# Kernel optimization log

Measured on AMD Instinct MI355X. Metric: run time of the kernel, lower is better.

The kernel has to match this reference:

```python
import jax, jax.numpy as jnp
import numpy as np


def setup_inputs() -> dict:
    key = jax.random.key(0)
    k1, k2, k3 = jax.random.split(key, 3)
    B, C, H, W, R = 4, 64, 128, 128, 16
    h_prev = jax.random.normal(k1, (B, C, H, W, R), dtype=jnp.float32)
    flow = jax.random.normal(k2, (B, 2, H, W), dtype=jnp.float32)
    dt = jax.random.uniform(k3, (B,), dtype=jnp.float32)
    return {"h_prev": h_prev, "flow": flow, "dt": dt}


def _bilinear_sample(img, ix, iy):
    # img: [K,H,W]; ix,iy: [H,W] unnormalized pixel coords, pre-clamped to
    # [0, W-1] / [0, H-1] (PyTorch grid_sample padding_mode='border').
    H, W = img.shape[-2], img.shape[-1]
    x0 = jnp.floor(ix)
    y0 = jnp.floor(iy)
    wx = ix - x0  # [H,W]
    wy = iy - y0
    x0i = jnp.clip(x0.astype(jnp.int32), 0, W - 1)
    x1i = jnp.clip(x0i + 1, 0, W - 1)
    y0i = jnp.clip(y0.astype(jnp.int32), 0, H - 1)
    y1i = jnp.clip(y0i + 1, 0, H - 1)
    v00 = img[:, y0i, x0i]  # [K,H,W]
    v01 = img[:, y0i, x1i]
    v10 = img[:, y1i, x0i]
    v11 = img[:, y1i, x1i]
    top = v00 * (1.0 - wx) + v01 * wx
    bot = v10 * (1.0 - wx) + v11 * wx
    return top * (1.0 - wy) + bot * wy


def reference(h_prev, flow, dt):
    B, C, H, W, R = h_prev.shape
    # base grid in normalized [-1,1] coords (torch.linspace endpoints)
    base_x = jnp.linspace(-1.0, 1.0, W, dtype=h_prev.dtype)[None, :]  # [1,W]
    base_y = jnp.linspace(-1.0, 1.0, H, dtype=h_prev.dtype)[:, None]  # [H,1]
    dtb = dt[:, None, None]  # [B,1,1]
    gx = base_x - flow[:, 0] * dtb  # [B,H,W] normalized x sample coords
    gy = base_y - flow[:, 1] * dtb  # [B,H,W]
    # unnormalize with align_corners=False, then border-clamp
    ix = jnp.clip(((gx + 1.0) * W - 1.0) * 0.5, 0.0, W - 1.0)
    iy = jnp.clip(((gy + 1.0) * H - 1.0) * 0.5, 0.0, H - 1.0)
    # grid is shared across R, so fold R into channels and sample once per batch
    img = jnp.moveaxis(h_prev, 4, 2).reshape(B, C * R, H, W)
    out = jax.vmap(_bilinear_sample)(img, ix, iy)  # [B, C*R, H, W]
    return jnp.moveaxis(out.reshape(B, C, R, H, W), 2, 4)  # [B,C,H,W,R]
```

## Files before the change

kernel.cpp:

```cpp
#include <hip/hip_runtime.h>


constexpr int B = 4, C = 64, H = 128, W = 128, R = 16;

__global__ __launch_bounds__(256) void lie_transport_kernel(
    const float* __restrict__ h_prev,
    const float* __restrict__ flow,
    const float* __restrict__ dt,
    float* __restrict__ out) {
  const int tid = blockIdx.x * 256 + threadIdx.x;
  const int r4  = (tid & 3) * 4;
  const int pix = tid >> 2;
  const int x = pix & (W - 1);
  const int y = (pix >> 7) & (H - 1);
  const int b = pix >> 14;

  const float dtb = dt[b];
  const float* fl = flow + (size_t)b * 2 * H * W;
  const float f0 = fl[y * W + x];
  const float f1 = fl[H * W + y * W + x];

  const float bx = -1.0f + 2.0f * (float)x / (float)(W - 1);
  const float by = -1.0f + 2.0f * (float)y / (float)(H - 1);
  const float gx = bx - f0 * dtb;
  const float gy = by - f1 * dtb;
  float ix = ((gx + 1.0f) * (float)W - 1.0f) * 0.5f;
  float iy = ((gy + 1.0f) * (float)H - 1.0f) * 0.5f;
  ix = fminf(fmaxf(ix, 0.0f), (float)(W - 1));
  iy = fminf(fmaxf(iy, 0.0f), (float)(H - 1));

  const float x0f = floorf(ix);
  const float y0f = floorf(iy);
  const float wx = ix - x0f;
  const float wy = iy - y0f;
  const int x0 = min(max((int)x0f, 0), W - 1);
  const int x1 = min(x0 + 1, W - 1);
  const int y0 = min(max((int)y0f, 0), H - 1);
  const int y1 = min(y0 + 1, H - 1);

  const float w00 = (1.0f - wx) * (1.0f - wy);
  const float w01 = wx * (1.0f - wy);
  const float w10 = (1.0f - wx) * wy;
  const float w11 = wx * wy;

  const size_t chwr = (size_t)H * W * R;
  const size_t base = (size_t)b * C * chwr;
  const size_t o00 = ((size_t)(y0 * W + x0)) * R + r4;
  const size_t o01 = ((size_t)(y0 * W + x1)) * R + r4;
  const size_t o10 = ((size_t)(y1 * W + x0)) * R + r4;
  const size_t o11 = ((size_t)(y1 * W + x1)) * R + r4;
  const size_t oou = ((size_t)(y  * W + x )) * R + r4;

#pragma unroll 4
  for (int c = 0; c < C; ++c) {
    const size_t cb = base + (size_t)c * chwr;
    const float4 v00 = *(const float4*)(h_prev + cb + o00);
    const float4 v01 = *(const float4*)(h_prev + cb + o01);
    const float4 v10 = *(const float4*)(h_prev + cb + o10);
    const float4 v11 = *(const float4*)(h_prev + cb + o11);
    float4 r;
    r.x = v00.x * w00 + v01.x * w01 + v10.x * w10 + v11.x * w11;
    r.y = v00.y * w00 + v01.y * w01 + v10.y * w10 + v11.y * w11;
    r.z = v00.z * w00 + v01.z * w01 + v10.z * w10 + v11.z * w11;
    r.w = v00.w * w00 + v01.w * w01 + v10.w * w10 + v11.w * w11;
    *(float4*)(out + cb + oou) = r;
  }
}

extern "C" void kernel_launch(void* const* d_in, const int* in_sizes, int n_in,
                              void* d_out, int out_size, void* d_ws, size_t ws_size,
                              hipStream_t stream) {
  const float* h_prev = (const float*)d_in[0];
  const float* flow   = (const float*)d_in[1];
  const float* dt     = (const float*)d_in[2];
  float* out = (float*)d_out;

  const int total_threads = B * H * W * 4;
  const int block = 256;
  const int grid = total_threads / block;
  lie_transport_kernel<<<grid, block, 0, stream>>>(h_prev, flow, dt, out);
}
```

Before: 540.9 us.

## Split channels across blocks with XCD-aware mapping and nontemporal stores

Each block now covers 64 pixels and only 2 channels instead of one thread looping over all 64 channels. The block index is remapped so each XCD keeps a contiguous set of (batch, channel) planes, which should localize gather reuse in that XCD's L2. Output is written with nontemporal stores so it does not evict input lines. In exchange the grid grows a lot and each thread recomputes the flow-derived coordinates and weights for every channel pair.

```diff
diff --git a/kernel.cpp b/kernel.cpp
--- a/kernel.cpp
+++ b/kernel.cpp
@@ -2,18 +2,33 @@
 
 
 constexpr int B = 4, C = 64, H = 128, W = 128, R = 16;
+constexpr int CH   = 2;
+constexpr int NXCD = 8;
+constexpr int PPB  = 64;
+constexpr int TILES  = (H * W) / PPB;
+constexpr int GROUPS = (B * C) / CH;
+
+typedef float nfloat4 __attribute__((ext_vector_type(4)));
 
 __global__ __launch_bounds__(256) void lie_transport_kernel(
     const float* __restrict__ h_prev,
     const float* __restrict__ flow,
     const float* __restrict__ dt,
     float* __restrict__ out) {
-  const int tid = blockIdx.x * 256 + threadIdx.x;
-  const int r4  = (tid & 3) * 4;
-  const int pix = tid >> 2;
+  const int blk  = blockIdx.x;
+  const int xcd  = blk & (NXCD - 1);
+  const int seq  = blk >> 3;
+  const int gidx = seq >> 8;
+  const int tile = seq & (TILES - 1);
+  const int pg   = gidx * NXCD + xcd;
+  const int b    = pg >> 5;
+  const int c0   = (pg & 31) * CH;
+
+  const int t   = threadIdx.x;
+  const int r4  = (t & 3) * 4;
+  const int pix = tile * PPB + (t >> 2);
   const int x = pix & (W - 1);
-  const int y = (pix >> 7) & (H - 1);
-  const int b = pix >> 14;
+  const int y = pix >> 7;
 
   const float dtb = dt[b];
   const float* fl = flow + (size_t)b * 2 * H * W;
@@ -44,26 +59,22 @@
   const float w11 = wx * wy;
 
   const size_t chwr = (size_t)H * W * R;
-  const size_t base = (size_t)b * C * chwr;
+  const size_t base = ((size_t)b * C + c0) * chwr;
   const size_t o00 = ((size_t)(y0 * W + x0)) * R + r4;
   const size_t o01 = ((size_t)(y0 * W + x1)) * R + r4;
   const size_t o10 = ((size_t)(y1 * W + x0)) * R + r4;
   const size_t o11 = ((size_t)(y1 * W + x1)) * R + r4;
   const size_t oou = ((size_t)(y  * W + x )) * R + r4;
 
-#pragma unroll 4
-  for (int c = 0; c < C; ++c) {
-    const size_t cb = base + (size_t)c * chwr;
-    const float4 v00 = *(const float4*)(h_prev + cb + o00);
-    const float4 v01 = *(const float4*)(h_prev + cb + o01);
-    const float4 v10 = *(const float4*)(h_prev + cb + o10);
-    const float4 v11 = *(const float4*)(h_prev + cb + o11);
-    float4 r;
-    r.x = v00.x * w00 + v01.x * w01 + v10.x * w10 + v11.x * w11;
-    r.y = v00.y * w00 + v01.y * w01 + v10.y * w10 + v11.y * w11;
-    r.z = v00.z * w00 + v01.z * w01 + v10.z * w10 + v11.z * w11;
-    r.w = v00.w * w00 + v01.w * w01 + v10.w * w10 + v11.w * w11;
-    *(float4*)(out + cb + oou) = r;
+#pragma unroll
+  for (int cc = 0; cc < CH; ++cc) {
+    const size_t cb = base + (size_t)cc * chwr;
+    const nfloat4 v00 = *(const nfloat4*)(h_prev + cb + o00);
+    const nfloat4 v01 = *(const nfloat4*)(h_prev + cb + o01);
+    const nfloat4 v10 = *(const nfloat4*)(h_prev + cb + o10);
+    const nfloat4 v11 = *(const nfloat4*)(h_prev + cb + o11);
+    nfloat4 r = v00 * w00 + v01 * w01 + v10 * w10 + v11 * w11;
+    __builtin_nontemporal_store(r, (nfloat4*)(out + cb + oou));
   }
 }
 
@@ -73,10 +84,8 @@
   const float* h_prev = (const float*)d_in[0];
   const float* flow   = (const float*)d_in[1];
   const float* dt     = (const float*)d_in[2];
-  float* out = (float*)d_out;
+  float* outp = (float*)d_out;
 
-  const int total_threads = B * H * W * 4;
-  const int block = 256;
-  const int grid = total_threads / block;
-  lie_transport_kernel<<<grid, block, 0, stream>>>(h_prev, flow, dt, out);
+  const int grid = GROUPS * TILES;
+  lie_transport_kernel<<<grid, 256, 0, stream>>>(h_prev, flow, dt, outp);
 }
```

New measurement: 482.1 us. 1.12x faster.
